# Kernel tuning notes

Hardware: AMD Instinct MI355X
Metric: run time of the kernel (lower is better)

Reference implementation:

```python
import jax, jax.numpy as jnp
from jax import lax
import numpy as np

B, C, L = 8, 64, 32768
K = 4
DEPTH = 8


def _causal_depthwise_conv(x, weight, dilation):
    # x: [B, C, L], weight: [C, 1, K] depthwise (groups=C). stride=1 so the
    # torch pad formula reduces to left-pad dilation*(K-1), output length L.
    pad = dilation * (K - 1)
    return lax.conv_general_dilated(
        x, weight,
        window_strides=(1,),
        padding=[(pad, 0)],
        rhs_dilation=(dilation,),
        dimension_numbers=("NCH", "OIH", "NCH"),
        feature_group_count=C,
    )


def setup_inputs() -> dict:
    key = jax.random.key(0)
    k1, k2, k3, k4 = jax.random.split(key, 4)
    scalar = np.sqrt(2.0 / (K * 2)).astype(np.float32)
    w_scale = np.sqrt(2.0 / (2 * DEPTH + 4)).astype(np.float32)
    return {
        "x": jax.random.normal(k1, (B, C, L), dtype=jnp.float32),
        "h0": jax.random.uniform(k2, (C, 1, K), minval=-1.0, maxval=1.0, dtype=jnp.float32) * scalar,
        "h1": jax.random.uniform(k3, (C, 1, K), minval=-1.0, maxval=1.0, dtype=jnp.float32) * scalar,
        "w": jax.random.uniform(k4, (C, DEPTH + 2), minval=-1.0, maxval=1.0, dtype=jnp.float32) * w_scale,
    }


def reference(x, h0, h1, w):
    residual_low = x
    y = jnp.zeros_like(x)
    dilation = 1
    for i in range(DEPTH, 0, -1):
        residual_high = _causal_depthwise_conv(residual_low, h1, dilation)
        residual_low = _causal_depthwise_conv(residual_low, h0, dilation)
        y = y + w[:, i][None, :, None] * residual_high
        dilation *= 2
    y = y + w[:, 0][None, :, None] * residual_low
    y = y + x * w[:, -1][None, :, None]
    # dropout p=0 is identity; torch GELU default is exact (erf)
    return jax.nn.gelu(y, approximate=False)
```

## Files before the change

### kernel.cpp

```cpp
#include <hip/hip_runtime.h>
#include <cmath>

namespace {

typedef _Float16 h8 __attribute__((ext_vector_type(8)));

constexpr int C_     = 64;
constexpr int L_     = 32768;
constexpr int TILE   = 4096;
constexpr int HALO   = 776;
constexpr int NB     = TILE + HALO;
constexpr int NU     = NB / 8;
constexpr int HALO_U = HALO / 8;
constexpr int NT     = L_ / TILE;
constexpr int BLK    = 256;
constexpr int UMAX   = (NU + BLK - 1) / BLK;

__device__ __forceinline__ h8 ld8(const _Float16* p) { return *reinterpret_cast<const h8*>(p); }
__device__ __forceinline__ void st8(_Float16* p, h8 v) { *reinterpret_cast<h8*>(p) = v; }
__device__ __forceinline__ float4 ld4f(const float* p) { return *reinterpret_cast<const float4*>(p); }
__device__ __forceinline__ void st4f(float* p, float4 v) { *reinterpret_cast<float4*>(p) = v; }
__device__ __forceinline__ h8 sp8(_Float16 v) { return (h8){v,v,v,v,v,v,v,v}; }

template<int K>
__device__ __forceinline__ h8 shconc(h8 A, h8 B) {
    return __builtin_shufflevector(A, B, K, K+1, K+2, K+3, K+4, K+5, K+6, K+7);
}

__device__ __forceinline__ float gelu_f(float v) {
    const float z = v * (1.5957691216057308f + 0.0713548162726f * v * v);
    const float e = __expf(-z);
    return v * __builtin_amdgcn_rcpf(1.0f + e);
}

template<int D, int STARTU, bool LAST>
__device__ __forceinline__ void level_pass(const _Float16* __restrict__ src,
                                           _Float16* __restrict__ dst,
                                           const float* h0f, const float* h1f,
                                           float wi, float w0,
                                           h8* lw, h8* yacc, int tid)
{
    _Float16 c1[4], c0[4];
#pragma unroll
    for (int t = 0; t < 4; ++t) {
        c1[t] = (_Float16)(wi * h1f[t]);
        c0[t] = (_Float16)(LAST ? w0 * h0f[t] : h0f[t]);
    }

#pragma unroll
    for (int u = 0; u < UMAX; ++u) {
        const int un = tid + u * BLK;
        if (un >= STARTU && un < NU) {
            const int p = 8 * un;
            const h8 T3 = lw[u];
            h8 T0, T1, T2;
            if constexpr (D == 1) {
                h8 Lv = ld8(&src[p - 8]);
                T0 = shconc<5>(Lv, T3);
                T1 = shconc<6>(Lv, T3);
                T2 = shconc<7>(Lv, T3);
            } else if constexpr (D == 2) {
                h8 Lv = ld8(&src[p - 8]);
                T0 = shconc<2>(Lv, T3);
                T1 = shconc<4>(Lv, T3);
                T2 = shconc<6>(Lv, T3);
            } else if constexpr (D == 4) {
                h8 Lv  = ld8(&src[p - 8]);
                h8 LL  = ld8(&src[p - 16]);
                T0 = shconc<4>(LL, Lv);
                T1 = Lv;
                T2 = shconc<4>(Lv, T3);
            } else {
                T0 = ld8(&src[p - 3 * D]);
                T1 = ld8(&src[p - 2 * D]);
                T2 = ld8(&src[p - D]);
            }
            if (un >= HALO_U) {
                yacc[u] += sp8(c1[0]) * T0 + sp8(c1[1]) * T1
                         + sp8(c1[2]) * T2 + sp8(c1[3]) * T3;
            }
            h8 nl = sp8(c0[0]) * T0 + sp8(c0[1]) * T1
                  + sp8(c0[2]) * T2 + sp8(c0[3]) * T3;
            if constexpr (LAST) {
                yacc[u] += nl;
            } else {
                lw[u] = nl;
                st8(&dst[p], nl);
            }
        }
    }
}

__global__ __launch_bounds__(BLK, 8)
void cmrc_kernel(const float* __restrict__ x,
                 const float* __restrict__ h0,
                 const float* __restrict__ h1,
                 const float* __restrict__ w,
                 float* __restrict__ out)
{
    __shared__ alignas(16) _Float16 buf[2][NB];

    const int tid  = threadIdx.x;
    const int blk  = blockIdx.x;
    const int tile = blk % NT;
    const int bc   = blk / NT;
    const int c    = bc % C_;
    const long row = (long)bc * L_;
    const int  t0  = tile * TILE - HALO;

    float h0v[4], h1v[4];
#pragma unroll
    for (int k = 0; k < 4; ++k) { h0v[k] = h0[c*4+k]; h1v[k] = h1[c*4+k]; }
    float wv[10];
#pragma unroll
    for (int i = 0; i < 10; ++i) wv[i] = w[c*10+i];

    h8 lw[UMAX];
    h8 yacc[UMAX];

    const _Float16 w9h = (_Float16)wv[9];

#pragma unroll
    for (int u = 0; u < UMAX; ++u) {
        yacc[u] = sp8((_Float16)0.f);
        const int un = tid + u * BLK;
        if (un < NU) {
            const int p = 8 * un;
            const int t = t0 + p;
            float4 xa = make_float4(0.f, 0.f, 0.f, 0.f);
            float4 xb = make_float4(0.f, 0.f, 0.f, 0.f);
            if (t >= 0)     xa = ld4f(&x[row + t]);
            if (t + 4 >= 0) xb = ld4f(&x[row + t + 4]);
            h8 hv;
            hv[0] = (_Float16)xa.x; hv[1] = (_Float16)xa.y;
            hv[2] = (_Float16)xa.z; hv[3] = (_Float16)xa.w;
            hv[4] = (_Float16)xb.x; hv[5] = (_Float16)xb.y;
            hv[6] = (_Float16)xb.z; hv[7] = (_Float16)xb.w;
            st8(&buf[0][p], hv);
            lw[u] = hv;
            if (un >= HALO_U) yacc[u] = sp8(w9h) * hv;
        }
    }
    __syncthreads();

    level_pass<1,   1,  false>(buf[0], buf[1], h0v, h1v, wv[8], 0.f, lw, yacc, tid); __syncthreads();
    level_pass<2,   2,  false>(buf[1], buf[0], h0v, h1v, wv[7], 0.f, lw, yacc, tid); __syncthreads();
    level_pass<4,   4,  false>(buf[0], buf[1], h0v, h1v, wv[6], 0.f, lw, yacc, tid); __syncthreads();
    level_pass<8,   7,  false>(buf[1], buf[0], h0v, h1v, wv[5], 0.f, lw, yacc, tid); __syncthreads();
    level_pass<16,  13, false>(buf[0], buf[1], h0v, h1v, wv[4], 0.f, lw, yacc, tid); __syncthreads();
    level_pass<32,  25, false>(buf[1], buf[0], h0v, h1v, wv[3], 0.f, lw, yacc, tid); __syncthreads();
    level_pass<64,  49, false>(buf[0], buf[1], h0v, h1v, wv[2], 0.f, lw, yacc, tid); __syncthreads();
    level_pass<128, 97, true >(buf[1], buf[0], h0v, h1v, wv[1], wv[0], lw, yacc, tid);

#pragma unroll
    for (int u = 0; u < UMAX; ++u) {
        const int un = tid + u * BLK;
        if (un >= HALO_U && un < NU) {
            const int p = 8 * un;
            const h8 v = yacc[u];
            float4 oa, ob;
            oa.x = gelu_f((float)v[0]); oa.y = gelu_f((float)v[1]);
            oa.z = gelu_f((float)v[2]); oa.w = gelu_f((float)v[3]);
            ob.x = gelu_f((float)v[4]); ob.y = gelu_f((float)v[5]);
            ob.z = gelu_f((float)v[6]); ob.w = gelu_f((float)v[7]);
            st4f(&out[row + t0 + p], oa);
            st4f(&out[row + t0 + p + 4], ob);
        }
    }
}

}

extern "C" void kernel_launch(void* const* d_in, const int* in_sizes, int n_in,
                              void* d_out, int out_size, void* d_ws, size_t ws_size,
                              hipStream_t stream)
{
    const float* x  = (const float*)d_in[0];
    const float* h0 = (const float*)d_in[1];
    const float* h1 = (const float*)d_in[2];
    const float* w  = (const float*)d_in[3];
    float* out = (float*)d_out;

    const int nblocks = (out_size / L_) * NT;
    cmrc_kernel<<<nblocks, BLK, 0, stream>>>(x, h0, h1, w, out);
}
```

Before: 45.57 us.

## Double tile size and use a single shared buffer with publish phases

Doubles the tile length so the 776-element halo recomputation is amortised over more output, and halves the blocks. The double-buffered shared array becomes a single buffer: each level computes into registers, syncs, writes its results back to shared memory, and syncs again. This keeps LDS use near the old footprint despite the larger tile, at the cost of an extra barrier per level and doubled per-thread register arrays (UMAX grows). It also lowers the launch-bounds occupancy hint from 8 to 7 and simplifies the halo load guard.

Result: no change. 46.06 us (+1.1%).

```diff
diff --git a/kernel.cpp b/kernel.cpp
--- a/kernel.cpp
+++ b/kernel.cpp
@@ -7,7 +7,7 @@
 
 constexpr int C_     = 64;
 constexpr int L_     = 32768;
-constexpr int TILE   = 4096;
+constexpr int TILE   = 8192;
 constexpr int HALO   = 776;
 constexpr int NB     = TILE + HALO;
 constexpr int NU     = NB / 8;
@@ -34,11 +34,10 @@
 }
 
 template<int D, int STARTU, bool LAST>
-__device__ __forceinline__ void level_pass(const _Float16* __restrict__ src,
-                                           _Float16* __restrict__ dst,
-                                           const float* h0f, const float* h1f,
-                                           float wi, float w0,
-                                           h8* lw, h8* yacc, int tid)
+__device__ __forceinline__ void level_compute(const _Float16* __restrict__ buf,
+                                              const float* h0f, const float* h1f,
+                                              float wi, float w0,
+                                              h8* lw, h8* yacc, int tid)
 {
     _Float16 c1[4], c0[4];
 #pragma unroll
@@ -55,25 +54,25 @@
             const h8 T3 = lw[u];
             h8 T0, T1, T2;
             if constexpr (D == 1) {
-                h8 Lv = ld8(&src[p - 8]);
+                h8 Lv = ld8(&buf[p - 8]);
                 T0 = shconc<5>(Lv, T3);
                 T1 = shconc<6>(Lv, T3);
                 T2 = shconc<7>(Lv, T3);
             } else if constexpr (D == 2) {
-                h8 Lv = ld8(&src[p - 8]);
+                h8 Lv = ld8(&buf[p - 8]);
                 T0 = shconc<2>(Lv, T3);
                 T1 = shconc<4>(Lv, T3);
                 T2 = shconc<6>(Lv, T3);
             } else if constexpr (D == 4) {
-                h8 Lv  = ld8(&src[p - 8]);
-                h8 LL  = ld8(&src[p - 16]);
+                h8 Lv  = ld8(&buf[p - 8]);
+                h8 LL  = ld8(&buf[p - 16]);
                 T0 = shconc<4>(LL, Lv);
                 T1 = Lv;
                 T2 = shconc<4>(Lv, T3);
             } else {
-                T0 = ld8(&src[p - 3 * D]);
-                T1 = ld8(&src[p - 2 * D]);
-                T2 = ld8(&src[p - D]);
+                T0 = ld8(&buf[p - 3 * D]);
+                T1 = ld8(&buf[p - 2 * D]);
+                T2 = ld8(&buf[p - D]);
             }
             if (un >= HALO_U) {
                 yacc[u] += sp8(c1[0]) * T0 + sp8(c1[1]) * T1
@@ -85,20 +84,30 @@
                 yacc[u] += nl;
             } else {
                 lw[u] = nl;
-                st8(&dst[p], nl);
             }
         }
     }
 }
 
-__global__ __launch_bounds__(BLK, 8)
+template<int STARTU>
+__device__ __forceinline__ void publish(_Float16* __restrict__ buf,
+                                        const h8* lw, int tid)
+{
+#pragma unroll
+    for (int u = 0; u < UMAX; ++u) {
+        const int un = tid + u * BLK;
+        if (un >= STARTU && un < NU) st8(&buf[8 * un], lw[u]);
+    }
+}
+
+__global__ __launch_bounds__(BLK, 7)
 void cmrc_kernel(const float* __restrict__ x,
                  const float* __restrict__ h0,
                  const float* __restrict__ h1,
                  const float* __restrict__ w,
                  float* __restrict__ out)
 {
-    __shared__ alignas(16) _Float16 buf[2][NB];
+    __shared__ alignas(16) _Float16 buf[NB];
 
     const int tid  = threadIdx.x;
     const int blk  = blockIdx.x;
@@ -129,28 +138,34 @@
             const int t = t0 + p;
             float4 xa = make_float4(0.f, 0.f, 0.f, 0.f);
             float4 xb = make_float4(0.f, 0.f, 0.f, 0.f);
-            if (t >= 0)     xa = ld4f(&x[row + t]);
-            if (t + 4 >= 0) xb = ld4f(&x[row + t + 4]);
+            if (t >= 0) { xa = ld4f(&x[row + t]); xb = ld4f(&x[row + t + 4]); }
             h8 hv;
             hv[0] = (_Float16)xa.x; hv[1] = (_Float16)xa.y;
             hv[2] = (_Float16)xa.z; hv[3] = (_Float16)xa.w;
             hv[4] = (_Float16)xb.x; hv[5] = (_Float16)xb.y;
             hv[6] = (_Float16)xb.z; hv[7] = (_Float16)xb.w;
-            st8(&buf[0][p], hv);
+            st8(&buf[p], hv);
             lw[u] = hv;
             if (un >= HALO_U) yacc[u] = sp8(w9h) * hv;
         }
     }
     __syncthreads();
 
-    level_pass<1,   1,  false>(buf[0], buf[1], h0v, h1v, wv[8], 0.f, lw, yacc, tid); __syncthreads();
-    level_pass<2,   2,  false>(buf[1], buf[0], h0v, h1v, wv[7], 0.f, lw, yacc, tid); __syncthreads();
-    level_pass<4,   4,  false>(buf[0], buf[1], h0v, h1v, wv[6], 0.f, lw, yacc, tid); __syncthreads();
-    level_pass<8,   7,  false>(buf[1], buf[0], h0v, h1v, wv[5], 0.f, lw, yacc, tid); __syncthreads();
-    level_pass<16,  13, false>(buf[0], buf[1], h0v, h1v, wv[4], 0.f, lw, yacc, tid); __syncthreads();
-    level_pass<32,  25, false>(buf[1], buf[0], h0v, h1v, wv[3], 0.f, lw, yacc, tid); __syncthreads();
-    level_pass<64,  49, false>(buf[0], buf[1], h0v, h1v, wv[2], 0.f, lw, yacc, tid); __syncthreads();
-    level_pass<128, 97, true >(buf[1], buf[0], h0v, h1v, wv[1], wv[0], lw, yacc, tid);
+#define LEVEL_STEP(D, SU, WI)                                                  \
+    level_compute<D, SU, false>(buf, h0v, h1v, WI, 0.f, lw, yacc, tid);        \
+    __syncthreads();                                                           \
+    publish<SU>(buf, lw, tid);                                                 \
+    __syncthreads();
+
+    LEVEL_STEP(1,   1,  wv[8])
+    LEVEL_STEP(2,   2,  wv[7])
+    LEVEL_STEP(4,   4,  wv[6])
+    LEVEL_STEP(8,   7,  wv[5])
+    LEVEL_STEP(16,  13, wv[4])
+    LEVEL_STEP(32,  25, wv[3])
+    LEVEL_STEP(64,  49, wv[2])
+#undef LEVEL_STEP
+    level_compute<128, 97, true>(buf, h0v, h1v, wv[1], wv[0], lw, yacc, tid);
 
 #pragma unroll
     for (int u = 0; u < UMAX; ++u) {
```
